# Kernel tuning notes

Measured on AMD Instinct MI355X. Metric: run time of the kernel, lower is better.

## Reference

```python
import jax, jax.numpy as jnp
import numpy as np

BN_EPS = 1e-5
NUM_SUBSET = 3


def setup_inputs() -> dict:
    key = jax.random.key(0)
    ks = jax.random.split(key, 6)
    N, C, T, V = 64, 192, 128, 25
    return {
        "x": jax.random.normal(ks[0], (N, C, T, V), dtype=jnp.float32),
        "Wqkv": jax.random.normal(ks[1], (3 * C, C), dtype=jnp.float32) * 0.05,
        "bqkv": jax.random.normal(ks[2], (3 * C,), dtype=jnp.float32) * 0.05,
        "Wff": jax.random.normal(ks[3], (C, C), dtype=jnp.float32) * 0.05,
        "bff": jax.random.normal(ks[4], (C,), dtype=jnp.float32) * 0.05,
        "gamma": jnp.ones((C,), dtype=jnp.float32),
        "beta": jnp.zeros((C,), dtype=jnp.float32),
        "running_mean": jnp.zeros((C,), dtype=jnp.float32),
        "running_var": jax.random.uniform(ks[5], (C,), dtype=jnp.float32) + 0.5,
    }


def reference(x, Wqkv, bqkv, Wff, bff, gamma, beta, running_mean, running_var):
    N, C, T, V = x.shape
    S = NUM_SUBSET
    mid = C // S  # mid_dim
    # 1x1 conv C -> 3C, then view (N, 3S, mid, T, V) and chunk into q,k,v
    qkv = jnp.einsum('nctv,oc->notv', x, Wqkv) + bqkv[None, :, None, None]
    qkv = qkv.reshape(N, 3 * S, mid, T, V)
    q, k, v = jnp.split(qkv, 3, axis=1)  # each (N, S, mid, T, V)
    # joint attention over V: contract channel and time, tanh instead of softmax
    att = jnp.tanh(jnp.einsum('nsctu,nsctv->nsuv', q, k) / (mid * T))  # (N,S,V,V)
    # weighted aggregation back to (N, C, T, V)
    y = jnp.einsum('nsuv,nsctv->nsctu', att, v).reshape(N, C, T, V)
    # ff_nets: 1x1 conv + BatchNorm2d (eval mode, running stats)
    y = jnp.einsum('nctv,oc->notv', y, Wff) + bff[None, :, None, None]
    inv = gamma / jnp.sqrt(running_var + BN_EPS)
    y = y * inv[None, :, None, None] + (beta - running_mean * inv)[None, :, None, None]
    # residual + LeakyReLU(0.1)
    out = jax.nn.leaky_relu(x + y, negative_slope=0.1)
    return (out, att)
```

## Files before the change

kernel.cpp:

```cpp
#include <hip/hip_runtime.h>
#include <hip/hip_bf16.h>

typedef __attribute__((ext_vector_type(8))) short bf16x8;
typedef __attribute__((ext_vector_type(4))) float f32x4;

#define MFMA16(a, b, c) __builtin_amdgcn_mfma_f32_16x16x32_bf16((a), (b), (c), 0, 0, 0)

#define N_ 64
#define C_ 192
#define T_ 128
#define V_ 25
#define S_ 3
#define MID 64
#define TV 3200
#define C3 576
#define OUT_ELEMS 39321600ULL
#define NCHUNK 16
#define PSTRIDE 640

static __device__ __forceinline__ float bf2f(ushort u) {
    union { unsigned int i; float f; } x; x.i = ((unsigned int)u) << 16; return x.f;
}
static __device__ __forceinline__ ushort f2bf(float f) {
    union { float f; unsigned int i; } x; x.f = f;
    unsigned int r = x.i + 0x7fffu + ((x.i >> 16) & 1u);
    return (ushort)(r >> 16);
}
static __device__ __forceinline__ unsigned int packcvt(float a, float b) {
    __hip_bfloat162 h = __float22bfloat162_rn(make_float2(a, b));
    union { __hip_bfloat162 h; unsigned int u; } c; c.h = h; return c.u;
}

__global__ __launch_bounds__(256) void kconv(const float* __restrict__ src,
                                             ushort* __restrict__ dst, int n4) {
    int i = blockIdx.x * 256 + threadIdx.x;
    if (i < n4) {
        float4 d = *(const float4*)(src + (size_t)i * 4);
        unsigned int* o = (unsigned int*)dst + (size_t)i * 2;
        o[0] = packcvt(d.x, d.y);
        o[1] = packcvt(d.z, d.w);
    }
}

__global__ __launch_bounds__(512, 4) void k1_qkv(const float* __restrict__ x,
                                                 const ushort* __restrict__ Wbf,
                                                 const float* __restrict__ bias,
                                                 ushort* __restrict__ qkvT) {
    int m0 = blockIdx.x * 128, n = blockIdx.y;
    __shared__ ushort As[2][64 * 200];
    __shared__ ushort Bs[64 * 200];
    __shared__ float biasS[C3];
    unsigned int* scratchU = (unsigned int*)Bs;
    ushort* scratchS = Bs;
    int tid = threadIdx.x;

    for (int i = tid; i < C3; i += 512) biasS[i] = bias[i];

    for (int h = 0; h < 2; h++) {
        for (int cg = 0; cg < 2; cg++) {
            if (h || cg) __syncthreads();
#pragma unroll
            for (int j = 0; j < 3; j++) {
                int chunk = tid + j * 512;
                int cc = chunk >> 4, m4 = chunk & 15;
                float4 d = *(const float4*)(x + ((size_t)n * C_ + cg * 96 + cc) * TV
                                            + m0 + h * 64 + m4 * 4);
                scratchU[cc * 35 + m4 * 2]     = packcvt(d.x, d.y);
                scratchU[cc * 35 + m4 * 2 + 1] = packcvt(d.z, d.w);
            }
            __syncthreads();
#pragma unroll
            for (int j = 0; j < 12; j++) {
                int idx = tid + j * 512;
                int mm = idx / 96, cc = idx % 96;
                As[h][mm * 200 + cg * 96 + cc] = scratchS[cc * 70 + mm];
            }
        }
    }
    __syncthreads();

    int wave = tid >> 6, lane = tid & 63;
    int h = wave >> 2, w4 = wave & 3;
    int mb = (w4 >> 1) * 32, ob = (w4 & 1) * 32;
    int lrow = lane & 15, lk = lane >> 4;
    const ushort* myAs = As[h];
    int mglob = m0 + h * 64;

    bf16x8 afrag[2][6];
#pragma unroll
    for (int ks = 0; ks < 6; ks++)
#pragma unroll
        for (int mt = 0; mt < 2; mt++)
            afrag[mt][ks] = *(const bf16x8*)&myAs[(mb + mt * 16 + lrow) * 200 + ks * 32 + lk * 8];

    for (int oi = 0; oi < 9; oi++) {
        int o0 = oi * 64;
        __syncthreads();
#pragma unroll
        for (int j = 0; j < 3; j++) {
            int chunk = tid + j * 512;
            int r = chunk / 24, c8 = chunk % 24;
            *(uint4*)&Bs[r * 200 + c8 * 8] =
                *(const uint4*)(Wbf + (size_t)(o0 + r) * C_ + c8 * 8);
        }
        __syncthreads();

        f32x4 acc[2][2];
#pragma unroll
        for (int i = 0; i < 2; i++)
#pragma unroll
            for (int j = 0; j < 2; j++) acc[i][j] = (f32x4){0.f, 0.f, 0.f, 0.f};

#pragma unroll
        for (int ks = 0; ks < 6; ks++) {
            bf16x8 b[2];
#pragma unroll
            for (int ot = 0; ot < 2; ot++)
                b[ot] = *(const bf16x8*)&Bs[(ob + ot * 16 + lrow) * 200 + ks * 32 + lk * 8];
#pragma unroll
            for (int mt = 0; mt < 2; mt++)
#pragma unroll
                for (int ot = 0; ot < 2; ot++)
                    acc[mt][ot] = MFMA16(afrag[mt][ks], b[ot], acc[mt][ot]);
        }

        ushort* op = qkvT + ((size_t)n * TV + mglob) * C3 + o0;
#pragma unroll
        for (int mt = 0; mt < 2; mt++) {
#pragma unroll
            for (int ot = 0; ot < 2; ot++) {
                int o = ob + ot * 16 + lrow;
                float bv = biasS[o0 + o];
                ushort* col = op + o;
#pragma unroll
                for (int r = 0; r < 4; r += 2) {
                    int m = mb + mt * 16 + lk * 4 + r;
                    unsigned int pk = packcvt(acc[mt][ot][r] + bv, acc[mt][ot][r + 1] + bv);
                    col[(size_t)m * C3] = (ushort)(pk & 0xffffu);
                    col[(size_t)(m + 1) * C3] = (ushort)(pk >> 16);
                }
            }
        }
    }
}

__global__ __launch_bounds__(256) void k2_att(const ushort* __restrict__ qkvT,
                                              float* __restrict__ partial) {
    int tc = blockIdx.x, s = blockIdx.y, n = blockIdx.z;
    __shared__ ushort tiles[4 * 2 * 32 * 72];
    __shared__ float red[4 * 32 * 33];
    int tid = threadIdx.x, wave = tid >> 6, lane = tid & 63;
    ushort* myQ = &tiles[wave * 2 * 2304];
    ushort* myK = myQ + 2304;

    if (lane < 63) {
        *(uint4*)&myQ[1800 + lane * 8] = (uint4){0, 0, 0, 0};
        *(uint4*)&myK[1800 + lane * 8] = (uint4){0, 0, 0, 0};
    }

    const size_t nbase = (size_t)n * TV * C3;
    int qoff = s * MID;
    int koff = C_ + s * MID;
    int lrow = lane & 15, lk = lane >> 4;

    f32x4 acc[2][2];
#pragma unroll
    for (int i = 0; i < 2; i++)
#pragma unroll
        for (int j = 0; j < 2; j++) acc[i][j] = (f32x4){0.f, 0.f, 0.f, 0.f};

#pragma unroll
    for (int i = 0; i < 2; i++) {
        int t = tc * 8 + wave + 4 * i;
#pragma unroll
        for (int j = 0; j < 7; j++) {
            int idx = lane + j * 64;
            if (idx < 400) {
                int op = idx / 200, rr = idx % 200;
                int row = rr >> 3, c16 = rr & 7;
                int chan = (op ? koff : qoff) + c16 * 8;
                uint4 d = *(const uint4*)(qkvT + nbase + (size_t)(t * V_ + row) * C3 + chan);
                *(uint4*)((op ? myK : myQ) + row * 72 + c16 * 8) = d;
            }
        }
#pragma unroll
        for (int ks = 0; ks < 2; ks++) {
            bf16x8 a0 = *(const bf16x8*)&myQ[lrow * 72 + ks * 32 + lk * 8];
            bf16x8 a1 = *(const bf16x8*)&myQ[(16 + lrow) * 72 + ks * 32 + lk * 8];
            bf16x8 b0 = *(const bf16x8*)&myK[lrow * 72 + ks * 32 + lk * 8];
            bf16x8 b1 = *(const bf16x8*)&myK[(16 + lrow) * 72 + ks * 32 + lk * 8];
            acc[0][0] = MFMA16(a0, b0, acc[0][0]);
            acc[0][1] = MFMA16(a0, b1, acc[0][1]);
            acc[1][0] = MFMA16(a1, b0, acc[1][0]);
            acc[1][1] = MFMA16(a1, b1, acc[1][1]);
        }
    }

#pragma unroll
    for (int ub = 0; ub < 2; ub++)
#pragma unroll
        for (int vb = 0; vb < 2; vb++)
#pragma unroll
            for (int r = 0; r < 4; r++) {
                int u = ub * 16 + lk * 4 + r, v = vb * 16 + lrow;
                red[wave * 1056 + u * 33 + v] = acc[ub][vb][r];
            }
    __syncthreads();

    float* pb = partial + (((size_t)n * S_ + s) * NCHUNK + tc) * PSTRIDE;
    for (int idx = tid; idx < 1024; idx += 256) {
        int u = idx >> 5, v = idx & 31;
        if (u < V_ && v < V_) {
            float sum = red[u * 33 + v] + red[1056 + u * 33 + v] +
                        red[2112 + u * 33 + v] + red[3168 + u * 33 + v];
            pb[u * V_ + v] = sum;
        }
    }
}

__global__ __launch_bounds__(256) void k2_reduce(const float* __restrict__ partial,
                                                 float* __restrict__ attOut) {
    int idx = blockIdx.x * 256 + threadIdx.x;
    if (idx >= 192 * 625) return;
    int ns = idx / 625, r = idx % 625;
    const float* p = partial + (size_t)ns * NCHUNK * PSTRIDE + r;
    float s = 0.f;
#pragma unroll
    for (int j = 0; j < NCHUNK; j++) s += p[j * PSTRIDE];
    attOut[(size_t)ns * 625 + r] = tanhf(s * (1.0f / 8192.0f));
}

__global__ __launch_bounds__(192) void k3_y(const ushort* __restrict__ qkvT,
                                            const float* __restrict__ attF,
                                            ushort* __restrict__ yT) {
    int t = blockIdx.x, n = blockIdx.y;
    __shared__ float attS[3 * 700];
    int tid = threadIdx.x;
    const float* ab = attF + (size_t)n * (S_ * V_ * V_);
    for (int idx = tid; idx < S_ * V_ * V_; idx += 192) {
        int s = idx / 625, r = idx % 625;
        attS[s * 700 + (r / 25) * 28 + (r % 25)] = ab[idx];
    }
    __syncthreads();

    int c = tid;
    int s = c >> 6;
    const ushort* vb = qkvT + ((size_t)n * TV + (size_t)t * V_) * C3 + 2 * C_ + c;
    float vreg[25];
#pragma unroll
    for (int v = 0; v < 25; v++) vreg[v] = bf2f(vb[(size_t)v * C3]);

    ushort* yb = yT + ((size_t)n * TV + (size_t)t * V_) * C_ + c;
    const float* as = &attS[s * 700];
    for (int u = 0; u < 25; u++) {
        float a = 0.f;
#pragma unroll
        for (int v = 0; v < 25; v++) a += as[u * 28 + v] * vreg[v];
        yb[(size_t)u * C_] = f2bf(a);
    }
}

__global__ __launch_bounds__(256, 3) void k4_out(const ushort* __restrict__ yT,
                                                 const ushort* __restrict__ Wbf,
                                                 const float* __restrict__ bff,
                                                 const float* __restrict__ gamma,
                                                 const float* __restrict__ beta,
                                                 const float* __restrict__ rmean,
                                                 const float* __restrict__ rvar,
                                                 const float* __restrict__ x,
                                                 float* __restrict__ out) {
    int m0 = blockIdx.x * 64, n = blockIdx.y;
    __shared__ ushort As[64 * 200];
    __shared__ ushort Bs[64 * 200];
    __shared__ float invS[C_], shiftS[C_];
    float* zT = (float*)Bs;
    int tid = threadIdx.x;

    const ushort* ab = yT + ((size_t)n * TV + m0) * C_;
#pragma unroll
    for (int j = 0; j < 6; j++) {
        int chunk = tid + j * 256;
        int r = chunk / 24, c8 = chunk % 24;
        *(uint4*)&As[r * 200 + c8 * 8] = *(const uint4*)(ab + (size_t)r * C_ + c8 * 8);
    }
    if (tid < C_) {
        float inv = gamma[tid] * rsqrtf(rvar[tid] + 1e-5f);
        invS[tid] = inv;
        shiftS[tid] = beta[tid] - rmean[tid] * inv + bff[tid] * inv;
    }
    __syncthreads();

    int wave = tid >> 6, lane = tid & 63;
    int mb = (wave >> 1) * 32, obw = (wave & 1) * 32;
    int lrow = lane & 15, lk = lane >> 4;

    bf16x8 afrag[2][6];
#pragma unroll
    for (int ks = 0; ks < 6; ks++)
#pragma unroll
        for (int mt = 0; mt < 2; mt++)
            afrag[mt][ks] = *(const bf16x8*)&As[(mb + mt * 16 + lrow) * 200 + ks * 32 + lk * 8];

    for (int oi = 0; oi < 3; oi++) {
        int o0 = oi * 64;
        __syncthreads();
#pragma unroll
        for (int j = 0; j < 6; j++) {
            int chunk = tid + j * 256;
            int r = chunk / 24, c8 = chunk % 24;
            *(uint4*)&Bs[r * 200 + c8 * 8] =
                *(const uint4*)(Wbf + (size_t)(o0 + r) * C_ + c8 * 8);
        }
        __syncthreads();

        f32x4 acc[2][2];
#pragma unroll
        for (int i = 0; i < 2; i++)
#pragma unroll
            for (int j = 0; j < 2; j++) acc[i][j] = (f32x4){0.f, 0.f, 0.f, 0.f};

#pragma unroll
        for (int ks = 0; ks < 6; ks++) {
            bf16x8 b[2];
#pragma unroll
            for (int ot = 0; ot < 2; ot++)
                b[ot] = *(const bf16x8*)&Bs[(obw + ot * 16 + lrow) * 200 + ks * 32 + lk * 8];
#pragma unroll
            for (int mt = 0; mt < 2; mt++)
#pragma unroll
                for (int ot = 0; ot < 2; ot++)
                    acc[mt][ot] = MFMA16(afrag[mt][ks], b[ot], acc[mt][ot]);
        }

        __syncthreads();
#pragma unroll
        for (int mt = 0; mt < 2; mt++)
#pragma unroll
            for (int ot = 0; ot < 2; ot++) {
                int o = obw + ot * 16 + lrow;
                float inv = invS[o0 + o], sh = shiftS[o0 + o];
#pragma unroll
                for (int r = 0; r < 4; r++) {
                    int m = mb + mt * 16 + lk * 4 + r;
                    zT[o * 68 + m] = acc[mt][ot][r] * inv + sh;
                }
            }
        __syncthreads();

        const float* xb = x + ((size_t)n * C_ + o0) * TV + m0;
        float* ob2 = out + ((size_t)n * C_ + o0) * TV + m0;
#pragma unroll
        for (int j = 0; j < 4; j++) {
            int chunk = tid + j * 256;
            int o = chunk >> 4, m4 = chunk & 15;
            float4 zv = *(float4*)&zT[o * 68 + m4 * 4];
            float4 xv = *(const float4*)(xb + (size_t)o * TV + m4 * 4);
            float4 res; float a;
            a = xv.x + zv.x; res.x = (a >= 0.f) ? a : 0.1f * a;
            a = xv.y + zv.y; res.y = (a >= 0.f) ? a : 0.1f * a;
            a = xv.z + zv.z; res.z = (a >= 0.f) ? a : 0.1f * a;
            a = xv.w + zv.w; res.w = (a >= 0.f) ? a : 0.1f * a;
            *(float4*)(ob2 + (size_t)o * TV + m4 * 4) = res;
        }
    }
}

extern "C" void kernel_launch(void* const* d_in, const int* in_sizes, int n_in,
                              void* d_out, int out_size, void* d_ws, size_t ws_size,
                              hipStream_t stream) {
    (void)in_sizes; (void)n_in; (void)out_size; (void)ws_size;
    const float* x    = (const float*)d_in[0];
    const float* Wqkv = (const float*)d_in[1];
    const float* bqkv = (const float*)d_in[2];
    const float* Wff  = (const float*)d_in[3];
    const float* bff  = (const float*)d_in[4];
    const float* gam  = (const float*)d_in[5];
    const float* bet  = (const float*)d_in[6];
    const float* rme  = (const float*)d_in[7];
    const float* rva  = (const float*)d_in[8];
    float* out = (float*)d_out;
    float* attOut = out + OUT_ELEMS;

    char* ws = (char*)d_ws;
    ushort* qkvT = (ushort*)ws;
    float*  partial = (float*)(ws + 235929600);
    ushort* yT      = (ushort*)(ws + 235929600);
    ushort* WqkvB   = (ushort*)(ws + 235929600);
    ushort* WffB    = (ushort*)ws;

    kconv<<<dim3(108), 256, 0, stream>>>(Wqkv, WqkvB, 27648);
    k1_qkv<<<dim3(25, 64), 512, 0, stream>>>(x, WqkvB, bqkv, qkvT);
    k2_att<<<dim3(NCHUNK, 3, 64), 256, 0, stream>>>(qkvT, partial);
    k2_reduce<<<dim3(469), 256, 0, stream>>>(partial, attOut);
    k3_y<<<dim3(128, 64), 192, 0, stream>>>(qkvT, attOut, yT);
    kconv<<<dim3(36), 256, 0, stream>>>(Wff, WffB, 9216);
    k4_out<<<dim3(50, 64), 256, 0, stream>>>(yT, WffB, bff, gam, bet, rme, rva, x, out);
}
```

Before: 481.3 us.

## Double-buffer weight tiles in QKV GEMM and read attention directly via scalar loads

In the QKV projection kernel, the next 64-row weight tile is prefetched into registers during the MFMA loop and written to an alternate LDS buffer (reusing the A staging area). This drops one barrier per iteration and hides the global load latency. In the aggregation kernel, the LDS staging of attention weights is removed. Each wave now reads its subset's attention matrix straight from global memory with a wave-uniform index, so the loads can become scalar, and the loop is reordered to accumulate 25 outputs in registers. The cost is higher register pressure in both kernels.

```diff
diff --git a/kernel.cpp b/kernel.cpp
--- a/kernel.cpp
+++ b/kernel.cpp
@@ -47,11 +47,12 @@
                                                  const float* __restrict__ bias,
                                                  ushort* __restrict__ qkvT) {
     int m0 = blockIdx.x * 128, n = blockIdx.y;
-    __shared__ ushort As[2][64 * 200];
-    __shared__ ushort Bs[64 * 200];
+    __shared__ __align__(16) ushort As[2][64 * 200];
+    __shared__ __align__(16) ushort Bs[64 * 200];
     __shared__ float biasS[C3];
     unsigned int* scratchU = (unsigned int*)Bs;
     ushort* scratchS = Bs;
+    ushort* BsAlt = (ushort*)As;
     int tid = threadIdx.x;
 
     for (int i = tid; i < C3; i += 512) biasS[i] = bias[i];
@@ -93,17 +94,35 @@
         for (int mt = 0; mt < 2; mt++)
             afrag[mt][ks] = *(const bf16x8*)&myAs[(mb + mt * 16 + lrow) * 200 + ks * 32 + lk * 8];
 
+    int sr[3], sc[3];
+#pragma unroll
+    for (int j = 0; j < 3; j++) {
+        int chunk = tid + j * 512;
+        sr[j] = chunk / 24; sc[j] = (chunk % 24) * 8;
+    }
+
+    {
+        uint4 st[3];
+#pragma unroll
+        for (int j = 0; j < 3; j++)
+            st[j] = *(const uint4*)(Wbf + (size_t)sr[j] * C_ + sc[j]);
+#pragma unroll
+        for (int j = 0; j < 3; j++)
+            *(uint4*)&Bs[sr[j] * 200 + sc[j]] = st[j];
+    }
+    __syncthreads();
+
     for (int oi = 0; oi < 9; oi++) {
         int o0 = oi * 64;
-        __syncthreads();
-#pragma unroll
-        for (int j = 0; j < 3; j++) {
-            int chunk = tid + j * 512;
-            int r = chunk / 24, c8 = chunk % 24;
-            *(uint4*)&Bs[r * 200 + c8 * 8] =
-                *(const uint4*)(Wbf + (size_t)(o0 + r) * C_ + c8 * 8);
-        }
-        __syncthreads();
+        const ushort* Bcur = (oi & 1) ? BsAlt : Bs;
+        ushort* Bnxt = (oi & 1) ? Bs : BsAlt;
+
+        uint4 st[3];
+        if (oi < 8) {
+#pragma unroll
+            for (int j = 0; j < 3; j++)
+                st[j] = *(const uint4*)(Wbf + (size_t)(o0 + 64 + sr[j]) * C_ + sc[j]);
+        }
 
         f32x4 acc[2][2];
 #pragma unroll
@@ -116,12 +135,18 @@
             bf16x8 b[2];
 #pragma unroll
             for (int ot = 0; ot < 2; ot++)
-                b[ot] = *(const bf16x8*)&Bs[(ob + ot * 16 + lrow) * 200 + ks * 32 + lk * 8];
+                b[ot] = *(const bf16x8*)&Bcur[(ob + ot * 16 + lrow) * 200 + ks * 32 + lk * 8];
 #pragma unroll
             for (int mt = 0; mt < 2; mt++)
 #pragma unroll
                 for (int ot = 0; ot < 2; ot++)
                     acc[mt][ot] = MFMA16(afrag[mt][ks], b[ot], acc[mt][ot]);
+        }
+
+        if (oi < 8) {
+#pragma unroll
+            for (int j = 0; j < 3; j++)
+                *(uint4*)&Bnxt[sr[j] * 200 + sc[j]] = st[j];
         }
 
         ushort* op = qkvT + ((size_t)n * TV + mglob) * C3 + o0;
@@ -141,6 +166,7 @@
                 }
             }
         }
+        __syncthreads();
     }
 }
 
@@ -234,30 +260,30 @@
                                             const float* __restrict__ attF,
                                             ushort* __restrict__ yT) {
     int t = blockIdx.x, n = blockIdx.y;
-    __shared__ float attS[3 * 700];
     int tid = threadIdx.x;
-    const float* ab = attF + (size_t)n * (S_ * V_ * V_);
-    for (int idx = tid; idx < S_ * V_ * V_; idx += 192) {
-        int s = idx / 625, r = idx % 625;
-        attS[s * 700 + (r / 25) * 28 + (r % 25)] = ab[idx];
-    }
-    __syncthreads();
-
     int c = tid;
-    int s = c >> 6;
+    int s = __builtin_amdgcn_readfirstlane(tid >> 6);
+    const float* __restrict__ as = attF + ((size_t)n * S_ + s) * 625;
+
     const ushort* vb = qkvT + ((size_t)n * TV + (size_t)t * V_) * C3 + 2 * C_ + c;
     float vreg[25];
 #pragma unroll
     for (int v = 0; v < 25; v++) vreg[v] = bf2f(vb[(size_t)v * C3]);
 
+    float acc[25];
+#pragma unroll
+    for (int u = 0; u < 25; u++) acc[u] = 0.f;
+
+#pragma unroll
+    for (int v = 0; v < 25; v++) {
+        float av = vreg[v];
+#pragma unroll
+        for (int u = 0; u < 25; u++) acc[u] += as[u * 25 + v] * av;
+    }
+
     ushort* yb = yT + ((size_t)n * TV + (size_t)t * V_) * C_ + c;
-    const float* as = &attS[s * 700];
-    for (int u = 0; u < 25; u++) {
-        float a = 0.f;
-#pragma unroll
-        for (int v = 0; v < 25; v++) a += as[u * 28 + v] * vreg[v];
-        yb[(size_t)u * C_] = f2bf(a);
-    }
+#pragma unroll
+    for (int u = 0; u < 25; u++) yb[(size_t)u * C_] = f2bf(acc[u]);
 }
 
 __global__ __launch_bounds__(256, 3) void k4_out(const ushort* __restrict__ yT,
@@ -270,8 +296,8 @@
                                                  const float* __restrict__ x,
                                                  float* __restrict__ out) {
     int m0 = blockIdx.x * 64, n = blockIdx.y;
-    __shared__ ushort As[64 * 200];
-    __shared__ ushort Bs[64 * 200];
+    __shared__ __align__(16) ushort As[64 * 200];
+    __shared__ __align__(16) ushort Bs[64 * 200];
     __shared__ float invS[C_], shiftS[C_];
     float* zT = (float*)Bs;
     int tid = threadIdx.x;
```

Result: no change. 488.4 us (+1.5%).
